# Performance work log

Measured on AMD Instinct MI355X. Metric: run time of the kernel, lower is better.

## Reference

```python
import jax, jax.numpy as jnp
import numpy as np

B, T, E = 32, 512, 256
H = 512          # num_cells
REV_H = 10       # hardcoded LSTM(10)
CONV_C = 60      # hardcoded Conv1D(60)
FEAT = 3 * CONV_C + REV_H  # 190
D0 = 100
TEMP = 1e-5
EPS = 1e-20


def setup_inputs() -> dict:
    key = jax.random.key(0)
    ks = jax.random.split(key, 18)
    def g(k, shape, fan_in):
        return (jax.random.normal(k, shape, jnp.float32) / np.float32(np.sqrt(fan_in)))
    inp = {}
    inp["x"] = jax.random.normal(ks[0], (B, T, E), jnp.float32)
    # Conv1D kernels in WIO layout [k, in, out]
    inp["conv1_w"] = g(ks[1], (3, E, CONV_C), 3 * E)
    inp["conv1_b"] = jnp.zeros((CONV_C,), jnp.float32)
    inp["conv2_w"] = g(ks[2], (4, E, CONV_C), 4 * E)
    inp["conv2_b"] = jnp.zeros((CONV_C,), jnp.float32)
    inp["conv3_w"] = g(ks[3], (5, E, CONV_C), 5 * E)
    inp["conv3_b"] = jnp.zeros((CONV_C,), jnp.float32)
    # reverse LSTM(10)
    inp["rev_Wx"] = g(ks[4], (E, 4 * REV_H), E)
    inp["rev_Wh"] = g(ks[5], (REV_H, 4 * REV_H), REV_H)
    inp["rev_b"] = jnp.zeros((4 * REV_H,), jnp.float32)
    # gate MLP: Dense(100, relu) -> Dense(2)
    inp["d0_W"] = g(ks[6], (FEAT + E, D0), FEAT + E)
    inp["d0_b"] = jnp.zeros((D0,), jnp.float32)
    inp["d1_W"] = g(ks[7], (D0, 2), D0)
    inp["d1_b"] = jnp.zeros((2,), jnp.float32)
    # main LSTMCell(H)
    inp["cell_Wx"] = g(ks[8], (E, 4 * H), E)
    inp["cell_Wh"] = g(ks[9], (H, 4 * H), H)
    inp["cell_b"] = jnp.zeros((4 * H,), jnp.float32)
    # pre-sampled Gumbel(0,1) noise, one per (t, b, 2)
    U = jax.random.uniform(ks[10], (T, B, 2), jnp.float32, 1e-7, 1.0)
    inp["gumbel_noise"] = -jnp.log(-jnp.log(U + EPS) + EPS)
    return inp


def _lstm_scan(xseq, Wx, Wh, b):
    # xseq: [T, B, E] -> hs: [T, B, H]
    h_dim = Wh.shape[0]
    bsz = xseq.shape[1]
    def step(carry, xt):
        h, c = carry
        z = xt @ Wx + h @ Wh + b
        i, f, g_, o = jnp.split(z, 4, axis=-1)
        c = jax.nn.sigmoid(f) * c + jax.nn.sigmoid(i) * jnp.tanh(g_)
        h = jax.nn.sigmoid(o) * jnp.tanh(c)
        return (h, c), h
    init = (jnp.zeros((bsz, h_dim), xseq.dtype), jnp.zeros((bsz, h_dim), xseq.dtype))
    _, hs = jax.lax.scan(step, init, xseq)
    return hs


def reference(x, conv1_w, conv1_b, conv2_w, conv2_b, conv3_w, conv3_b,
              rev_Wx, rev_Wh, rev_b, d0_W, d0_b, d1_W, d1_b,
              cell_Wx, cell_Wh, cell_b, gumbel_noise):
    dn = ('NWC', 'WIO', 'NWC')
    def conv(w, b_):
        return jax.lax.conv_general_dilated(x, w, (1,), 'SAME', dimension_numbers=dn) + b_
    conved = jnp.concatenate([conv(conv1_w, conv1_b), conv(conv2_w, conv2_b), conv(conv3_w, conv3_b)], axis=-1)  # [B,T,180]
    # LSTM over reversed sequence (output NOT re-reversed, as in the original)
    x_rev = x[:, ::-1, :].transpose(1, 0, 2)               # [T,B,E]
    rev = _lstm_scan(x_rev, rev_Wx, rev_Wh, rev_b).transpose(1, 0, 2)  # [B,T,10]
    f_core = jnp.concatenate([conved, rev], axis=-1)        # [B,T,190]
    # f_all[:, t+1] for t in [0,T): shift left by one, pad a zero row at the end
    ff_seq = jnp.concatenate([f_core[:, 1:, :], jnp.zeros_like(f_core[:, :1, :])], axis=1)  # [B,T,190]

    bsz = x.shape[0]
    h_dim = cell_Wh.shape[0]
    xs = (x.transpose(1, 0, 2), ff_seq.transpose(1, 0, 2), gumbel_noise)

    def step(carry, inputs):
        h, c = carry
        xt, ff, gn = inputs
        # skip-gate logits -> Gumbel-softmax (temperature 1e-5)
        hid = jax.nn.relu(jnp.concatenate([ff, xt], axis=-1) @ d0_W + d0_b)
        pi = hid @ d1_W + d1_b                               # [B,2]
        d = jax.nn.softmax((pi + gn) / TEMP, axis=-1)        # [B,2]
        # LSTM cell candidate
        z = xt @ cell_Wx + h @ cell_Wh + cell_b
        i, f, g_, o = jnp.split(z, 4, axis=-1)
        c_cand = jax.nn.sigmoid(f) * c + jax.nn.sigmoid(i) * jnp.tanh(g_)
        h_cand = jax.nn.sigmoid(o) * jnp.tanh(c_cand)
        d0, d1 = d[:, :1], d[:, 1:]
        h_new = d0 * h_cand + d1 * h
        c_new = d0 * c_cand + d1 * c
        # output written each step is the (ungated) candidate h, per the source
        return (h_new, c_new), h_cand

    init = (jnp.zeros((bsz, h_dim), x.dtype), jnp.zeros((bsz, h_dim), x.dtype))
    _, outs = jax.lax.scan(step, init, xs)                  # [T,B,H]
    return outs.transpose(1, 0, 2)                          # [B,T,H]
```

## Files before the change

### kernel.cpp

```cpp
#include <hip/hip_runtime.h>
#include <math.h>

#define Bz 32
#define Tz 512
#define Ez 256
#define Hz 512
#define FCH 446

__device__ __forceinline__ float sigf(float x){ return 1.0f/(1.0f + __expf(-x)); }
__device__ __forceinline__ float tanhfast(float x){ return 1.0f - 2.0f/(__expf(2.0f*x) + 1.0f); }

__global__ __launch_bounds__(256) void k_conv(
    const float* __restrict__ x,
    const float* __restrict__ w1, const float* __restrict__ b1,
    const float* __restrict__ w2, const float* __restrict__ b2,
    const float* __restrict__ w3, const float* __restrict__ b3,
    const float* __restrict__ rwx,
    float* __restrict__ feat, float* __restrict__ rxw)
{
  __shared__ __align__(16) float xs[256*40];
  int b  = blockIdx.x >> 4;
  int t0 = (blockIdx.x & 15) * 32;
  int tid = threadIdx.x;
  for (int i = 0; i < 36; ++i){
    int t = t0 - 2 + i;
    xs[tid*40 + i] = (t >= 0 && t < Tz) ? x[(b*Tz + t)*Ez + tid] : 0.0f;
  }
  __syncthreads();
  for (int i = 0; i < 32; ++i){
    int t = t0 + i;
    feat[((size_t)t*Bz + b)*FCH + 190 + tid] = xs[tid*40 + i + 2];
  }
  int tq = tid & 7, cs = tid >> 3;
  float acc[6][4];
  float racc[2][4];
  #pragma unroll
  for (int ci = 0; ci < 6; ++ci){
    int c = cs + 32*ci;
    float bv = 0.0f;
    if (c < 60) bv = b1[c];
    else if (c < 120) bv = b2[c-60];
    else if (c < 180) bv = b3[c-120];
    acc[ci][0]=acc[ci][1]=acc[ci][2]=acc[ci][3]=bv;
  }
  #pragma unroll
  for (int ji = 0; ji < 2; ++ji){ racc[ji][0]=racc[ji][1]=racc[ji][2]=racc[ji][3]=0.0f; }

  for (int e = 0; e < 256; ++e){
    const float* xr = &xs[e*40 + 4*tq];
    float4 wa = *(const float4*)(xr);
    float4 wb = *(const float4*)(xr + 4);
    float wd[8] = {wa.x, wa.y, wa.z, wa.w, wb.x, wb.y, wb.z, wb.w};
    #pragma unroll
    for (int ci = 0; ci < 6; ++ci){
      int c = cs + 32*ci;
      if (c < 60){
        #pragma unroll
        for (int k = 0; k < 3; ++k){
          float wv = w1[(k*256 + e)*60 + c];
          #pragma unroll
          for (int j = 0; j < 4; ++j) acc[ci][j] = fmaf(wd[1 + j + k], wv, acc[ci][j]);
        }
      } else if (c < 120){
        int cc = c - 60;
        #pragma unroll
        for (int k = 0; k < 4; ++k){
          float wv = w2[(k*256 + e)*60 + cc];
          #pragma unroll
          for (int j = 0; j < 4; ++j) acc[ci][j] = fmaf(wd[1 + j + k], wv, acc[ci][j]);
        }
      } else if (c < 180){
        int cc = c - 120;
        #pragma unroll
        for (int k = 0; k < 5; ++k){
          float wv = w3[(k*256 + e)*60 + cc];
          #pragma unroll
          for (int j = 0; j < 4; ++j) acc[ci][j] = fmaf(wd[j + k], wv, acc[ci][j]);
        }
      }
    }
    #pragma unroll
    for (int ji = 0; ji < 2; ++ji){
      int jc = cs + 32*ji;
      if (jc < 40){
        float wv = rwx[e*40 + jc];
        #pragma unroll
        for (int j = 0; j < 4; ++j) racc[ji][j] = fmaf(wd[2 + j], wv, racc[ji][j]);
      }
    }
  }
  #pragma unroll
  for (int ci = 0; ci < 6; ++ci){
    int c = cs + 32*ci;
    if (c < 180){
      #pragma unroll
      for (int j = 0; j < 4; ++j){
        int t = t0 + 4*tq + j;
        if (t >= 1) feat[((size_t)(t-1)*Bz + b)*FCH + c] = acc[ci][j];
      }
    }
  }
  #pragma unroll
  for (int ji = 0; ji < 2; ++ji){
    int jc = cs + 32*ji;
    if (jc < 40){
      #pragma unroll
      for (int j = 0; j < 4; ++j){
        int t = t0 + 4*tq + j;
        rxw[((size_t)(511 - t)*Bz + b)*40 + jc] = racc[ji][j];
      }
    }
  }
}

__global__ __launch_bounds__(64) void k_rev(const float* __restrict__ rxw,
    const float* __restrict__ revWh, const float* __restrict__ revb, float* __restrict__ feat){
  int b = blockIdx.x;
  int j = threadIdx.x;
  float wreg[10];
  float bias = 0.0f;
  #pragma unroll
  for (int k = 0; k < 10; ++k) wreg[k] = 0.0f;
  if (j < 40){
    bias = revb[j];
    #pragma unroll
    for (int k = 0; k < 10; ++k) wreg[k] = revWh[k*40 + j];
  }
  float h[10];
  #pragma unroll
  for (int k = 0; k < 10; ++k) h[k] = 0.0f;
  float c = 0.0f;
  for (int s = 0; s < Tz; ++s){
    float z = bias + ((j < 40) ? rxw[(s*Bz + b)*40 + j] : 0.0f);
    #pragma unroll
    for (int k = 0; k < 10; ++k) z = fmaf(h[k], wreg[k], z);
    float a = (j >= 20 && j < 30) ? tanhfast(z) : sigf(z);
    float af = __shfl(a, j + 10);
    float ag = __shfl(a, j + 20);
    float ao = __shfl(a, j + 30);
    if (j < 10) c = af*c + a*ag;
    float hn = ao * tanhfast(c);
    #pragma unroll
    for (int k = 0; k < 10; ++k) h[k] = __shfl(hn, k);
    if (j < 10 && s >= 1) feat[((size_t)(s-1)*Bz + b)*FCH + 180 + j] = hn;
  }
}

__global__ __launch_bounds__(256) void k_hid(const float* __restrict__ feat,
    const float* __restrict__ d0W, const float* __restrict__ d0b, float* __restrict__ hid){
  __shared__ __align__(16) float fT[446*36];
  int r0 = blockIdx.x * 32;
  int tid = threadIdx.x;
  for (int r = 0; r < 32; ++r){
    fT[tid*36 + r] = feat[(size_t)(r0 + r)*FCH + tid];
    if (tid < 190) fT[(tid + 256)*36 + r] = feat[(size_t)(r0 + r)*FCH + tid + 256];
  }
  __syncthreads();
  int cs = tid & 31, rq = tid >> 5;
  if (cs < 25){
    float4 accv[4];
    #pragma unroll
    for (int jc = 0; jc < 4; ++jc) accv[jc] = make_float4(0.f,0.f,0.f,0.f);
    for (int k = 0; k < 446; ++k){
      float4 xv = *(const float4*)&fT[k*36 + 4*rq];
      float4 wv = *(const float4*)&d0W[k*100 + 4*cs];
      accv[0].x = fmaf(xv.x, wv.x, accv[0].x); accv[0].y = fmaf(xv.y, wv.x, accv[0].y);
      accv[0].z = fmaf(xv.z, wv.x, accv[0].z); accv[0].w = fmaf(xv.w, wv.x, accv[0].w);
      accv[1].x = fmaf(xv.x, wv.y, accv[1].x); accv[1].y = fmaf(xv.y, wv.y, accv[1].y);
      accv[1].z = fmaf(xv.z, wv.y, accv[1].z); accv[1].w = fmaf(xv.w, wv.y, accv[1].w);
      accv[2].x = fmaf(xv.x, wv.z, accv[2].x); accv[2].y = fmaf(xv.y, wv.z, accv[2].y);
      accv[2].z = fmaf(xv.z, wv.z, accv[2].z); accv[2].w = fmaf(xv.w, wv.z, accv[2].w);
      accv[3].x = fmaf(xv.x, wv.w, accv[3].x); accv[3].y = fmaf(xv.y, wv.w, accv[3].y);
      accv[3].z = fmaf(xv.z, wv.w, accv[3].z); accv[3].w = fmaf(xv.w, wv.w, accv[3].w);
    }
    #pragma unroll
    for (int i = 0; i < 4; ++i){
      int row = r0 + 4*rq + i;
      float4 o;
      float vi[4] = { i==0?accv[0].x:(i==1?accv[0].y:(i==2?accv[0].z:accv[0].w)),
                      i==0?accv[1].x:(i==1?accv[1].y:(i==2?accv[1].z:accv[1].w)),
                      i==0?accv[2].x:(i==1?accv[2].y:(i==2?accv[2].z:accv[2].w)),
                      i==0?accv[3].x:(i==1?accv[3].y:(i==2?accv[3].z:accv[3].w)) };
      o.x = fmaxf(vi[0] + d0b[4*cs+0], 0.0f);
      o.y = fmaxf(vi[1] + d0b[4*cs+1], 0.0f);
      o.z = fmaxf(vi[2] + d0b[4*cs+2], 0.0f);
      o.w = fmaxf(vi[3] + d0b[4*cs+3], 0.0f);
      *(float4*)&hid[(size_t)row*100 + 4*cs] = o;
    }
  }
}

__global__ __launch_bounds__(128) void k_pi(const float* __restrict__ hid,
    const float* __restrict__ d1W, const float* __restrict__ d1b,
    const float* __restrict__ gum, float* __restrict__ d0a, float* __restrict__ d1a){
  __shared__ float hidL[64*100];
  int r0 = blockIdx.x * 64;
  int tid = threadIdx.x;
  for (int i = 0; i < 50; ++i) hidL[tid + 128*i] = hid[(size_t)r0*100 + tid + 128*i];
  __syncthreads();
  int r = tid >> 1, pp = tid & 1;
  float s = d1b[pp];
  for (int m = 0; m < 100; ++m) s = fmaf(hidL[r*100 + m], d1W[m*2 + pp], s);
  int row = r0 + r;
  float a = (s + gum[row*2 + pp]) / 1e-5f;
  float other = __shfl_xor(a, 1);
  float mx = fmaxf(a, other);
  float ea = expf(a - mx), eb = expf(other - mx);
  float d = ea / (ea + eb);
  if (pp == 0) d0a[row] = d; else d1a[row] = d;
}

__global__ __launch_bounds__(256) void k_xz(const float* __restrict__ x,
    const float* __restrict__ Wx, const float* __restrict__ cb, float* __restrict__ xzG){
  __shared__ __align__(16) float xT[256*36];
  int t  = blockIdx.x & 511;
  int c0 = (blockIdx.x >> 9) * 128;
  int tid = threadIdx.x;
  for (int b = 0; b < 32; ++b){
    xT[tid*36 + b] = x[(b*Tz + t)*Ez + tid];
  }
  __syncthreads();
  int cs = tid & 31, rq = tid >> 5;
  float4 accv[4];
  #pragma unroll
  for (int jc = 0; jc < 4; ++jc) accv[jc] = make_float4(0.f,0.f,0.f,0.f);
  float4 wv = *(const float4*)&Wx[c0 + 4*cs];
  for (int e = 0; e < 256; ++e){
    float4 wc = wv;
    if (e != 255) wv = *(const float4*)&Wx[(e+1)*2048 + c0 + 4*cs];
    float4 xv = *(const float4*)&xT[e*36 + 4*rq];
    accv[0].x = fmaf(xv.x, wc.x, accv[0].x); accv[0].y = fmaf(xv.y, wc.x, accv[0].y);
    accv[0].z = fmaf(xv.z, wc.x, accv[0].z); accv[0].w = fmaf(xv.w, wc.x, accv[0].w);
    accv[1].x = fmaf(xv.x, wc.y, accv[1].x); accv[1].y = fmaf(xv.y, wc.y, accv[1].y);
    accv[1].z = fmaf(xv.z, wc.y, accv[1].z); accv[1].w = fmaf(xv.w, wc.y, accv[1].w);
    accv[2].x = fmaf(xv.x, wc.z, accv[2].x); accv[2].y = fmaf(xv.y, wc.z, accv[2].y);
    accv[2].z = fmaf(xv.z, wc.z, accv[2].z); accv[2].w = fmaf(xv.w, wc.z, accv[2].w);
    accv[3].x = fmaf(xv.x, wc.w, accv[3].x); accv[3].y = fmaf(xv.y, wc.w, accv[3].y);
    accv[3].z = fmaf(xv.z, wc.w, accv[3].z); accv[3].w = fmaf(xv.w, wc.w, accv[3].w);
  }
  #pragma unroll
  for (int jc = 0; jc < 4; ++jc){
    int col = c0 + 4*cs + jc;
    float bv = cb[col];
    float4 o = accv[jc];
    o.x += bv; o.y += bv; o.z += bv; o.w += bv;
    *(float4*)&xzG[(((size_t)rq*Tz + t)*2048 + col)*4] = o;
  }
}

__global__ __launch_bounds__(512, 2) void k_scan(
    const float* __restrict__ Wh, const float* __restrict__ xzG,
    const float* __restrict__ d0a, const float* __restrict__ d1a,
    float* __restrict__ hG,
    unsigned int* __restrict__ tags,
    float* __restrict__ out)
{
  __shared__ __align__(16) float hL[4*520];
  __shared__ __align__(16) float part[8*260];
  __shared__ float zL[256];
  __shared__ float hcandL[64];
  __shared__ float dv0L[2048];
  __shared__ float dv1L[2048];

  int tid = threadIdx.x;
  int g = blockIdx.x & 7;
  int m = blockIdx.x >> 3;
  int w = tid >> 6;
  int lane = tid & 63;

  float wreg[8][8];
  {
    int colbase = ((w >> 1) << 9) + (m << 4) + ((w & 1) << 3);
    #pragma unroll
    for (int j = 0; j < 8; ++j){
      const float4* wp = (const float4*)(Wh + (size_t)(lane*8 + j)*2048 + colbase);
      float4 a = wp[0], bq = wp[1];
      wreg[0][j]=a.x;  wreg[1][j]=a.y;  wreg[2][j]=a.z;  wreg[3][j]=a.w;
      wreg[4][j]=bq.x; wreg[5][j]=bq.y; wreg[6][j]=bq.z; wreg[7][j]=bq.w;
    }
  }
  for (int i = tid; i < 2048; i += 512){
    int tt = i >> 2, bb = i & 3;
    dv0L[i] = d0a[tt*32 + (g << 2) + bb];
    dv1L[i] = d1a[tt*32 + (g << 2) + bb];
  }

  int q0 = 2*lane;
  int sw = (q0 >> 3) & 3;
  int p0 = ((q0  ) ^ sw) << 2;
  int p1 = ((q0+1) ^ sw) << 2;

  int stb = tid >> 7, stq = tid & 127;
  int stp = (stq ^ ((stq >> 3) & 3)) << 2;
  const int hrow = 520;
  const unsigned int* mytag = tags + (g << 5) + (stq >> 2);

  int rcg = tid >> 2, rb = tid & 3;
  int rcol = ((rcg >> 4) << 9) + (m << 4) + (rcg & 15);
  size_t xzbase = ((size_t)g*Tz)*8192 + (size_t)rcol*4 + rb;

  float* hg0 = hG + (size_t)(g*2 + 0) * (4*512);
  float* hg1 = hG + (size_t)(g*2 + 1) * (4*512);

  float c_reg = 0.0f;
  float h_reg = 0.0f;

  for (int t = 0; t < Tz; ++t){
    const float* hcur = (t & 1) ? hg1 : hg0;
    float*       hnxt = (t & 1) ? hg0 : hg1;

    if (t == 0){
      *(float4*)&hL[stb*hrow + stp] = make_float4(0.f,0.f,0.f,0.f);
    } else {
      while (__hip_atomic_load(mytag, __ATOMIC_RELAXED, __HIP_MEMORY_SCOPE_AGENT)
             < (unsigned)t) { }
      const float* src = hcur + stb*512 + stq*4;
      float4 v;
      v.x = __hip_atomic_load(src+0, __ATOMIC_RELAXED, __HIP_MEMORY_SCOPE_AGENT);
      v.y = __hip_atomic_load(src+1, __ATOMIC_RELAXED, __HIP_MEMORY_SCOPE_AGENT);
      v.z = __hip_atomic_load(src+2, __ATOMIC_RELAXED, __HIP_MEMORY_SCOPE_AGENT);
      v.w = __hip_atomic_load(src+3, __ATOMIC_RELAXED, __HIP_MEMORY_SCOPE_AGENT);
      *(float4*)&hL[stb*hrow + stp] = v;
    }
    float xzv = 0.0f;
    if (tid < 256) xzv = xzG[xzbase + (size_t)t*8192];
    __syncthreads();

    float acc[8][4];
    #pragma unroll
    for (int ci = 0; ci < 8; ++ci)
      #pragma unroll
      for (int b = 0; b < 4; ++b) acc[ci][b] = 0.0f;
    #pragma unroll
    for (int b = 0; b < 4; ++b){
      const float* hr = &hL[b*hrow];
      float4 h0 = *(const float4*)(hr + p0);
      float4 h1 = *(const float4*)(hr + p1);
      float hv[8] = {h0.x,h0.y,h0.z,h0.w,h1.x,h1.y,h1.z,h1.w};
      #pragma unroll
      for (int j = 0; j < 8; ++j){
        #pragma unroll
        for (int ci = 0; ci < 8; ++ci)
          acc[ci][b] = fmaf(wreg[ci][j], hv[j], acc[ci][b]);
      }
    }

    float v16[16];
    {
      bool hi = (lane & 1);
      #pragma unroll
      for (int i = 0; i < 16; ++i){
        int ci = i >> 2, b = i & 3;
        float keep = hi ? acc[4+ci][b] : acc[ci][b];
        float send = hi ? acc[ci][b]   : acc[4+ci][b];
        v16[i] = keep + __shfl_xor(send, 1);
      }
    }
    float v8[8];
    {
      bool hi = (lane & 2);
      #pragma unroll
      for (int i = 0; i < 8; ++i){
        float keep = hi ? v16[8+i] : v16[i];
        float send = hi ? v16[i]   : v16[8+i];
        v8[i] = keep + __shfl_xor(send, 2);
      }
    }
    float v4[4];
    {
      bool hi = (lane & 4);
      #pragma unroll
      for (int b = 0; b < 4; ++b){
        float keep = hi ? v8[4+b] : v8[b];
        float send = hi ? v8[b]   : v8[4+b];
        v4[b] = keep + __shfl_xor(send, 4);
      }
    }
    {
      int e = ((lane & 1) << 2) | (lane & 2) | ((lane >> 2) & 1);
      float* pw = &part[(lane >> 3)*260 + ((8*w + e) << 2)];
      *(float4*)pw = make_float4(v4[0], v4[1], v4[2], v4[3]);
    }
    __syncthreads();

    if (tid < 256){
      float s0 = part[0*260 + tid] + part[1*260 + tid];
      float s1 = part[2*260 + tid] + part[3*260 + tid];
      float s2 = part[4*260 + tid] + part[5*260 + tid];
      float s3 = part[6*260 + tid] + part[7*260 + tid];
      zL[tid] = (s0+s1)+(s2+s3) + xzv;
    }
    __syncthreads();

    if (tid < 64){
      int jl = tid >> 2, bb = tid & 3;
      float zi = zL[      (jl << 2) + bb];
      float zf = zL[ 64 + (jl << 2) + bb];
      float zg = zL[128 + (jl << 2) + bb];
      float zo = zL[192 + (jl << 2) + bb];
      float dv0 = dv0L[(t << 2) + bb];
      float dv1 = dv1L[(t << 2) + bb];
      int hk = (m << 4) + jl;
      float ccand = sigf(zf)*c_reg + sigf(zi)*tanhfast(zg);
      float hcand = sigf(zo)*tanhfast(ccand);
      c_reg = dv0*ccand + dv1*c_reg;
      float hnew = dv0*hcand + dv1*h_reg;
      h_reg = hnew;
      hcandL[(bb << 4) + jl] = hcand;
      __hip_atomic_store(hnxt + bb*512 + hk, hnew,
                         __ATOMIC_RELAXED, __HIP_MEMORY_SCOPE_AGENT);
      asm volatile("s_waitcnt vmcnt(0)" ::: "memory");
      if (tid == 0){
        __hip_atomic_store(tags + (g << 5) + m, (unsigned)(t+1),
                           __ATOMIC_RELAXED, __HIP_MEMORY_SCOPE_AGENT);
      }
    }
    __syncthreads();

    if (tid >= 64 && tid < 80){
      int idx = tid - 64; int bb = idx >> 2, q = idx & 3;
      float4 v = *(const float4*)&hcandL[(bb << 4) + 4*q];
      *(float4*)(out + (size_t)((g << 2) + bb)*(Tz*Hz) + (size_t)t*Hz + (m << 4) + 4*q) = v;
    }
  }
}

extern "C" void kernel_launch(void* const* d_in, const int* in_sizes, int n_in,
                              void* d_out, int out_size, void* d_ws, size_t ws_size,
                              hipStream_t stream)
{
  const float* x       = (const float*)d_in[0];
  const float* conv1_w = (const float*)d_in[1];
  const float* conv1_b = (const float*)d_in[2];
  const float* conv2_w = (const float*)d_in[3];
  const float* conv2_b = (const float*)d_in[4];
  const float* conv3_w = (const float*)d_in[5];
  const float* conv3_b = (const float*)d_in[6];
  const float* rev_Wx  = (const float*)d_in[7];
  const float* rev_Wh  = (const float*)d_in[8];
  const float* rev_b   = (const float*)d_in[9];
  const float* d0_W    = (const float*)d_in[10];
  const float* d0_b    = (const float*)d_in[11];
  const float* d1_W    = (const float*)d_in[12];
  const float* d1_b    = (const float*)d_in[13];
  const float* cell_Wx = (const float*)d_in[14];
  const float* cell_Wh = (const float*)d_in[15];
  const float* cell_b  = (const float*)d_in[16];
  const float* gumbel  = (const float*)d_in[17];
  float* out = (float*)d_out;

  char* ws = (char*)d_ws;
  size_t off = 0;
  float* xzG  = (float*)(ws + off); off += (size_t)Tz*2048*Bz*4;
  float* feat = (float*)(ws + off); off += (size_t)Tz*Bz*FCH*4;
  float* rxw  = (float*)(ws + off); off += (size_t)Tz*Bz*40*4;
  float* hid  = (float*)(ws + off); off += (size_t)Tz*Bz*100*4;
  float* d0a  = (float*)(ws + off); off += (size_t)Tz*Bz*4;
  float* d1a  = (float*)(ws + off); off += (size_t)Tz*Bz*4;
  float* hG   = (float*)(ws + off); off += (size_t)8*2*4*512*4;
  unsigned int* tags = (unsigned int*)(ws + off); off += 8*32*4;

  hipMemsetAsync(feat + (size_t)(Tz-1)*Bz*FCH, 0, Bz*FCH*4, stream);
  hipMemsetAsync(tags, 0, 8*32*4, stream);

  k_conv<<<512, 256, 0, stream>>>(x, conv1_w, conv1_b, conv2_w, conv2_b,
                                  conv3_w, conv3_b, rev_Wx, feat, rxw);
  k_rev<<<32, 64, 0, stream>>>(rxw, rev_Wh, rev_b, feat);
  k_hid<<<512, 256, 0, stream>>>(feat, d0_W, d0_b, hid);
  k_pi<<<256, 128, 0, stream>>>(hid, d1_W, d1_b, gumbel, d0a, d1a);
  k_xz<<<8192, 256, 0, stream>>>(x, cell_Wx, cell_b, xzG);

  k_scan<<<256, 512, 0, stream>>>(cell_Wh, xzG, d0a, d1a, hG, tags, out);
}
```

Before: 3.219 ms.

## Fuse preprocessing kernels into one persistent kernel with atomic work queue

Merges the conv, reverse-LSTM, hidden-MLP, gate and input-projection kernels into a single persistent 256-block kernel. Blocks pull units from an atomic counter, so the serial reverse-LSTM in 32 blocks can overlap with the input-projection GEMM units running on the other blocks. The hid and pi steps are fused through shared memory, which removes the hid buffer from global memory. The reverse LSTM now prefetches the next input, and the scan's tag publish moves after the barrier instead of waiting on vmcnt. The spin-wait dependencies rely on all 256 blocks being co-resident.

```diff
diff --git a/kernel.cpp b/kernel.cpp
--- a/kernel.cpp
+++ b/kernel.cpp
@@ -10,18 +10,16 @@
 __device__ __forceinline__ float sigf(float x){ return 1.0f/(1.0f + __expf(-x)); }
 __device__ __forceinline__ float tanhfast(float x){ return 1.0f - 2.0f/(__expf(2.0f*x) + 1.0f); }
 
-__global__ __launch_bounds__(256) void k_conv(
+
+__device__ __forceinline__ void conv_unit(int b, int tt, int tid,
     const float* __restrict__ x,
     const float* __restrict__ w1, const float* __restrict__ b1,
     const float* __restrict__ w2, const float* __restrict__ b2,
     const float* __restrict__ w3, const float* __restrict__ b3,
     const float* __restrict__ rwx,
-    float* __restrict__ feat, float* __restrict__ rxw)
-{
-  __shared__ __align__(16) float xs[256*40];
-  int b  = blockIdx.x >> 4;
-  int t0 = (blockIdx.x & 15) * 32;
-  int tid = threadIdx.x;
+    float* __restrict__ feat, float* __restrict__ rxw, float* xs)
+{
+  int t0 = tt * 32;
   for (int i = 0; i < 36; ++i){
     int t = t0 - 2 + i;
     xs[tid*40 + i] = (t >= 0 && t < Tz) ? x[(b*Tz + t)*Ez + tid] : 0.0f;
@@ -111,12 +109,13 @@
       }
     }
   }
-}
-
-__global__ __launch_bounds__(64) void k_rev(const float* __restrict__ rxw,
-    const float* __restrict__ revWh, const float* __restrict__ revb, float* __restrict__ feat){
-  int b = blockIdx.x;
-  int j = threadIdx.x;
+  __syncthreads();
+}
+
+__device__ __forceinline__ void rev_unit(int b, int j,
+    const float* __restrict__ rxw, const float* __restrict__ revWh,
+    const float* __restrict__ revb, float* __restrict__ feat)
+{
   float wreg[10];
   float bias = 0.0f;
   #pragma unroll
@@ -130,8 +129,11 @@
   #pragma unroll
   for (int k = 0; k < 10; ++k) h[k] = 0.0f;
   float c = 0.0f;
+  float zin = (j < 40) ? rxw[(0*Bz + b)*40 + j] : 0.0f;
   for (int s = 0; s < Tz; ++s){
-    float z = bias + ((j < 40) ? rxw[(s*Bz + b)*40 + j] : 0.0f);
+    float zcur = zin;
+    if (s < Tz-1 && j < 40) zin = rxw[((s+1)*Bz + b)*40 + j];
+    float z = bias + zcur;
     #pragma unroll
     for (int k = 0; k < 10; ++k) z = fmaf(h[k], wreg[k], z);
     float a = (j >= 20 && j < 30) ? tanhfast(z) : sigf(z);
@@ -146,14 +148,18 @@
   }
 }
 
-__global__ __launch_bounds__(256) void k_hid(const float* __restrict__ feat,
-    const float* __restrict__ d0W, const float* __restrict__ d0b, float* __restrict__ hid){
-  __shared__ __align__(16) float fT[446*36];
-  int r0 = blockIdx.x * 32;
-  int tid = threadIdx.x;
+__device__ __forceinline__ void hidpi_unit(int t, int tid,
+    const float* __restrict__ feat,
+    const float* __restrict__ d0W, const float* __restrict__ d0b,
+    const float* __restrict__ d1W, const float* __restrict__ d1b,
+    const float* __restrict__ gum,
+    float* __restrict__ d0a, float* __restrict__ d1a,
+    float* fT, float* hidT)
+{
+  size_t r0 = (size_t)t * 32;
   for (int r = 0; r < 32; ++r){
-    fT[tid*36 + r] = feat[(size_t)(r0 + r)*FCH + tid];
-    if (tid < 190) fT[(tid + 256)*36 + r] = feat[(size_t)(r0 + r)*FCH + tid + 256];
+    fT[tid*36 + r] = feat[(r0 + r)*FCH + tid];
+    if (tid < 190) fT[(tid + 256)*36 + r] = feat[(r0 + r)*FCH + tid + 256];
   }
   __syncthreads();
   int cs = tid & 31, rq = tid >> 5;
@@ -175,7 +181,7 @@
     }
     #pragma unroll
     for (int i = 0; i < 4; ++i){
-      int row = r0 + 4*rq + i;
+      int rl = 4*rq + i;
       float4 o;
       float vi[4] = { i==0?accv[0].x:(i==1?accv[0].y:(i==2?accv[0].z:accv[0].w)),
                       i==0?accv[1].x:(i==1?accv[1].y:(i==2?accv[1].z:accv[1].w)),
@@ -185,66 +191,123 @@
       o.y = fmaxf(vi[1] + d0b[4*cs+1], 0.0f);
       o.z = fmaxf(vi[2] + d0b[4*cs+2], 0.0f);
       o.w = fmaxf(vi[3] + d0b[4*cs+3], 0.0f);
-      *(float4*)&hid[(size_t)row*100 + 4*cs] = o;
-    }
-  }
-}
-
-__global__ __launch_bounds__(128) void k_pi(const float* __restrict__ hid,
+      *(float4*)&hidT[rl*104 + 4*cs] = o;
+    }
+  }
+  __syncthreads();
+  if (tid < 64){
+    int r = tid >> 1, pp = tid & 1;
+    float s = d1b[pp];
+    for (int m2 = 0; m2 < 100; ++m2) s = fmaf(hidT[r*104 + m2], d1W[m2*2 + pp], s);
+    size_t row = r0 + r;
+    float a = (s + gum[row*2 + pp]) / 1e-5f;
+    float other = __shfl_xor(a, 1);
+    float mx = fmaxf(a, other);
+    float ea = expf(a - mx), eb = expf(other - mx);
+    float d = ea / (ea + eb);
+    if (pp == 0) d0a[row] = d; else d1a[row] = d;
+  }
+  __syncthreads();
+}
+
+__device__ __forceinline__ void xz_unit(int t, int q, int tid,
+    const float* __restrict__ x, const float* __restrict__ Wx,
+    const float* __restrict__ cb, float* __restrict__ xzG, float* xT)
+{
+  for (int bb = 0; bb < 32; ++bb)
+    xT[tid*36 + bb] = x[(bb*Tz + t)*Ez + tid];
+  __syncthreads();
+  int cs = tid & 31, rq = tid >> 5;
+  for (int c0i = 4*q; c0i < 4*q + 4; ++c0i){
+    int c0 = c0i * 128;
+    float4 accv[4];
+    #pragma unroll
+    for (int jc = 0; jc < 4; ++jc) accv[jc] = make_float4(0.f,0.f,0.f,0.f);
+    float4 wv = *(const float4*)&Wx[c0 + 4*cs];
+    for (int e = 0; e < 256; ++e){
+      float4 wc = wv;
+      if (e != 255) wv = *(const float4*)&Wx[(e+1)*2048 + c0 + 4*cs];
+      float4 xv = *(const float4*)&xT[e*36 + 4*rq];
+      accv[0].x = fmaf(xv.x, wc.x, accv[0].x); accv[0].y = fmaf(xv.y, wc.x, accv[0].y);
+      accv[0].z = fmaf(xv.z, wc.x, accv[0].z); accv[0].w = fmaf(xv.w, wc.x, accv[0].w);
+      accv[1].x = fmaf(xv.x, wc.y, accv[1].x); accv[1].y = fmaf(xv.y, wc.y, accv[1].y);
+      accv[1].z = fmaf(xv.z, wc.y, accv[1].z); accv[1].w = fmaf(xv.w, wc.y, accv[1].w);
+      accv[2].x = fmaf(xv.x, wc.z, accv[2].x); accv[2].y = fmaf(xv.y, wc.z, accv[2].y);
+      accv[2].z = fmaf(xv.z, wc.z, accv[2].z); accv[2].w = fmaf(xv.w, wc.z, accv[2].w);
+      accv[3].x = fmaf(xv.x, wc.w, accv[3].x); accv[3].y = fmaf(xv.y, wc.w, accv[3].y);
+      accv[3].z = fmaf(xv.z, wc.w, accv[3].z); accv[3].w = fmaf(xv.w, wc.w, accv[3].w);
+    }
+    #pragma unroll
+    for (int jc = 0; jc < 4; ++jc){
+      int col = c0 + 4*cs + jc;
+      float bv = cb[col];
+      float4 o = accv[jc];
+      o.x += bv; o.y += bv; o.z += bv; o.w += bv;
+      *(float4*)&xzG[(((size_t)rq*Tz + t)*2048 + col)*4] = o;
+    }
+  }
+  __syncthreads();
+}
+
+__global__ __launch_bounds__(256) void k_pre(
+    const float* __restrict__ x,
+    const float* __restrict__ w1, const float* __restrict__ b1,
+    const float* __restrict__ w2, const float* __restrict__ b2,
+    const float* __restrict__ w3, const float* __restrict__ b3,
+    const float* __restrict__ revWx, const float* __restrict__ revWh,
+    const float* __restrict__ revb,
+    const float* __restrict__ d0W, const float* __restrict__ d0b,
     const float* __restrict__ d1W, const float* __restrict__ d1b,
-    const float* __restrict__ gum, float* __restrict__ d0a, float* __restrict__ d1a){
-  __shared__ float hidL[64*100];
-  int r0 = blockIdx.x * 64;
-  int tid = threadIdx.x;
-  for (int i = 0; i < 50; ++i) hidL[tid + 128*i] = hid[(size_t)r0*100 + tid + 128*i];
-  __syncthreads();
-  int r = tid >> 1, pp = tid & 1;
-  float s = d1b[pp];
-  for (int m = 0; m < 100; ++m) s = fmaf(hidL[r*100 + m], d1W[m*2 + pp], s);
-  int row = r0 + r;
-  float a = (s + gum[row*2 + pp]) / 1e-5f;
-  float other = __shfl_xor(a, 1);
-  float mx = fmaxf(a, other);
-  float ea = expf(a - mx), eb = expf(other - mx);
-  float d = ea / (ea + eb);
-  if (pp == 0) d0a[row] = d; else d1a[row] = d;
-}
-
-__global__ __launch_bounds__(256) void k_xz(const float* __restrict__ x,
-    const float* __restrict__ Wx, const float* __restrict__ cb, float* __restrict__ xzG){
-  __shared__ __align__(16) float xT[256*36];
-  int t  = blockIdx.x & 511;
-  int c0 = (blockIdx.x >> 9) * 128;
-  int tid = threadIdx.x;
-  for (int b = 0; b < 32; ++b){
-    xT[tid*36 + b] = x[(b*Tz + t)*Ez + tid];
-  }
-  __syncthreads();
-  int cs = tid & 31, rq = tid >> 5;
-  float4 accv[4];
-  #pragma unroll
-  for (int jc = 0; jc < 4; ++jc) accv[jc] = make_float4(0.f,0.f,0.f,0.f);
-  float4 wv = *(const float4*)&Wx[c0 + 4*cs];
-  for (int e = 0; e < 256; ++e){
-    float4 wc = wv;
-    if (e != 255) wv = *(const float4*)&Wx[(e+1)*2048 + c0 + 4*cs];
-    float4 xv = *(const float4*)&xT[e*36 + 4*rq];
-    accv[0].x = fmaf(xv.x, wc.x, accv[0].x); accv[0].y = fmaf(xv.y, wc.x, accv[0].y);
-    accv[0].z = fmaf(xv.z, wc.x, accv[0].z); accv[0].w = fmaf(xv.w, wc.x, accv[0].w);
-    accv[1].x = fmaf(xv.x, wc.y, accv[1].x); accv[1].y = fmaf(xv.y, wc.y, accv[1].y);
-    accv[1].z = fmaf(xv.z, wc.y, accv[1].z); accv[1].w = fmaf(xv.w, wc.y, accv[1].w);
-    accv[2].x = fmaf(xv.x, wc.z, accv[2].x); accv[2].y = fmaf(xv.y, wc.z, accv[2].y);
-    accv[2].z = fmaf(xv.z, wc.z, accv[2].z); accv[2].w = fmaf(xv.w, wc.z, accv[2].w);
-    accv[3].x = fmaf(xv.x, wc.w, accv[3].x); accv[3].y = fmaf(xv.y, wc.w, accv[3].y);
-    accv[3].z = fmaf(xv.z, wc.w, accv[3].z); accv[3].w = fmaf(xv.w, wc.w, accv[3].w);
-  }
-  #pragma unroll
-  for (int jc = 0; jc < 4; ++jc){
-    int col = c0 + 4*cs + jc;
-    float bv = cb[col];
-    float4 o = accv[jc];
-    o.x += bv; o.y += bv; o.z += bv; o.w += bv;
-    *(float4*)&xzG[(((size_t)rq*Tz + t)*2048 + col)*4] = o;
+    const float* __restrict__ Wx, const float* __restrict__ cbias,
+    const float* __restrict__ gum,
+    float* __restrict__ feat, float* __restrict__ rxw,
+    float* __restrict__ d0a, float* __restrict__ d1a,
+    float* __restrict__ xzG,
+    unsigned int* __restrict__ cnt)
+{
+  __shared__ __align__(16) float sm[19384];
+  __shared__ unsigned smu;
+  int tid = threadIdx.x, bid = blockIdx.x;
+
+  for (int u = bid; u < 512; u += 256){
+    conv_unit(u >> 4, u & 15, tid, x, w1, b1, w2, b2, w3, b3, revWx, feat, rxw, sm);
+    if (tid == 0){
+      __threadfence();
+      __hip_atomic_fetch_add(&cnt[u >> 4], 1u, __ATOMIC_RELAXED, __HIP_MEMORY_SCOPE_AGENT);
+    }
+  }
+
+  if (bid < 32){
+    while (__hip_atomic_load(&cnt[bid], __ATOMIC_RELAXED, __HIP_MEMORY_SCOPE_AGENT) < 16u) {}
+    __threadfence();
+    __syncthreads();
+    if (tid < 64) rev_unit(bid, tid, rxw, revWh, revb, feat);
+    __syncthreads();
+    if (tid == 0){
+      __threadfence();
+      __hip_atomic_fetch_add(&cnt[32], 1u, __ATOMIC_RELAXED, __HIP_MEMORY_SCOPE_AGENT);
+    }
+  }
+
+  bool gated = false;
+  for (;;){
+    if (tid == 0)
+      smu = __hip_atomic_fetch_add(&cnt[33], 1u, __ATOMIC_RELAXED, __HIP_MEMORY_SCOPE_AGENT);
+    __syncthreads();
+    unsigned u = smu;
+    if (u >= 2560u) break;
+    if (u < 2048u){
+      xz_unit((int)(u >> 2), (int)(u & 3), tid, x, Wx, cbias, xzG, sm);
+    } else {
+      if (!gated){
+        while (__hip_atomic_load(&cnt[32], __ATOMIC_RELAXED, __HIP_MEMORY_SCOPE_AGENT) < 32u) {}
+        __threadfence();
+        __syncthreads();
+        gated = true;
+      }
+      hidpi_unit((int)(u - 2048u), tid, feat, d0W, d0b, d1W, d1b, gum,
+                 d0a, d1a, sm, sm + 16056);
+    }
   }
 }
 
@@ -409,14 +472,13 @@
       hcandL[(bb << 4) + jl] = hcand;
       __hip_atomic_store(hnxt + bb*512 + hk, hnew,
                          __ATOMIC_RELAXED, __HIP_MEMORY_SCOPE_AGENT);
-      asm volatile("s_waitcnt vmcnt(0)" ::: "memory");
-      if (tid == 0){
-        __hip_atomic_store(tags + (g << 5) + m, (unsigned)(t+1),
-                           __ATOMIC_RELAXED, __HIP_MEMORY_SCOPE_AGENT);
-      }
-    }
-    __syncthreads();
-
+    }
+    __syncthreads();
+
+    if (tid == 0){
+      __hip_atomic_store(tags + (g << 5) + m, (unsigned)(t+1),
+                         __ATOMIC_RELAXED, __HIP_MEMORY_SCOPE_AGENT);
+    }
     if (tid >= 64 && tid < 80){
       int idx = tid - 64; int bb = idx >> 2, q = idx & 3;
       float4 v = *(const float4*)&hcandL[(bb << 4) + 4*q];
@@ -454,21 +516,19 @@
   float* xzG  = (float*)(ws + off); off += (size_t)Tz*2048*Bz*4;
   float* feat = (float*)(ws + off); off += (size_t)Tz*Bz*FCH*4;
   float* rxw  = (float*)(ws + off); off += (size_t)Tz*Bz*40*4;
-  float* hid  = (float*)(ws + off); off += (size_t)Tz*Bz*100*4;
   float* d0a  = (float*)(ws + off); off += (size_t)Tz*Bz*4;
   float* d1a  = (float*)(ws + off); off += (size_t)Tz*Bz*4;
   float* hG   = (float*)(ws + off); off += (size_t)8*2*4*512*4;
   unsigned int* tags = (unsigned int*)(ws + off); off += 8*32*4;
+  unsigned int* cnt  = (unsigned int*)(ws + off); off += 64*4;
 
   hipMemsetAsync(feat + (size_t)(Tz-1)*Bz*FCH, 0, Bz*FCH*4, stream);
-  hipMemsetAsync(tags, 0, 8*32*4, stream);
-
-  k_conv<<<512, 256, 0, stream>>>(x, conv1_w, conv1_b, conv2_w, conv2_b,
-                                  conv3_w, conv3_b, rev_Wx, feat, rxw);
-  k_rev<<<32, 64, 0, stream>>>(rxw, rev_Wh, rev_b, feat);
-  k_hid<<<512, 256, 0, stream>>>(feat, d0_W, d0_b, hid);
-  k_pi<<<256, 128, 0, stream>>>(hid, d1_W, d1_b, gumbel, d0a, d1a);
-  k_xz<<<8192, 256, 0, stream>>>(x, cell_Wx, cell_b, xzG);
+  hipMemsetAsync(tags, 0, 8*32*4 + 64*4, stream);
+
+  k_pre<<<256, 256, 0, stream>>>(x, conv1_w, conv1_b, conv2_w, conv2_b,
+                                 conv3_w, conv3_b, rev_Wx, rev_Wh, rev_b,
+                                 d0_W, d0_b, d1_W, d1_b, cell_Wx, cell_b, gumbel,
+                                 feat, rxw, d0a, d1a, xzG, cnt);
 
   k_scan<<<256, 512, 0, stream>>>(cell_Wh, xzG, d0a, d1a, hG, tags, out);
 }
```

After: 3.002 ms. 6.8% less time.
